# Performance work log

Measured on AMD Instinct MI355X. Metric: run time of the kernel, lower is better.

The kernel has to match this reference:

```python
import jax, jax.numpy as jnp
import numpy as np

VOCAB = 1024
D = 1024  # predictor_dim
B = 32
U = 512
NULL_INDEX = 0


def setup_inputs() -> dict:
    key = jax.random.key(0)
    ks = jax.random.split(key, 9)
    s = 1.0 / np.sqrt(D)
    return {
        "y": jax.random.randint(ks[0], (B, U), 0, VOCAB, dtype=jnp.int32),
        "embed_table": jax.random.normal(ks[1], (VOCAB, D), jnp.float32) * s,
        "Wx": jax.random.normal(ks[2], (D, 3 * D), jnp.float32) * s,  # input kernel [z|r|h]
        "Wh": jax.random.normal(ks[3], (D, 3 * D), jnp.float32) * s,  # recurrent kernel [z|r|h]
        "bx": jnp.zeros((3 * D,), jnp.float32),  # input bias (reset_after=True)
        "bh": jnp.zeros((3 * D,), jnp.float32),  # recurrent bias (reset_after=True)
        "Wd": jax.random.normal(ks[4], (D, D), jnp.float32) * s,
        "bd": jnp.zeros((D,), jnp.float32),
        "h0": jax.random.normal(ks[5], (D,), jnp.float32),  # self.initial_state
    }


def _gru_scan(tokens, embed_table, Wx, Wh, bx, bh, h0_b):
    # tokens: [B, T] int; returns hidden states [B, T, D]
    x = embed_table[tokens]                       # [B, T, D]
    # Precompute all input projections outside the recurrence (one big GEMM)
    xp = jnp.einsum("btd,de->bte", x, Wx) + bx    # [B, T, 3D]
    xp = jnp.moveaxis(xp, 1, 0)                   # [T, B, 3D]

    def step(h, xp_t):
        hp = h @ Wh + bh                          # [B, 3D], reset_after=True
        xz, xr, xh = jnp.split(xp_t, 3, axis=-1)
        hz, hr, hh = jnp.split(hp, 3, axis=-1)
        z = jax.nn.sigmoid(xz + hz)
        r = jax.nn.sigmoid(xr + hr)
        hcand = jnp.tanh(xh + r * hh)
        h_new = z * h + (1.0 - z) * hcand
        return h_new, h_new

    _, hs = jax.lax.scan(step, h0_b, xp)          # hs: [T, B, D]
    return jnp.moveaxis(hs, 0, 1)                 # [B, T, D]


def reference(y, embed_table, Wx, Wh, bx, bh, Wd, bd, h0):
    Bn = y.shape[0]
    start = jnp.full((Bn, 1), NULL_INDEX, dtype=y.dtype)
    tokens = jnp.concatenate([start, y], axis=1)  # [B, U+1]
    h0_b = jnp.broadcast_to(h0, (Bn, D))
    hs = _gru_scan(tokens, embed_table, Wx, Wh, bx, bh, h0_b)  # [B, U+1, D]
    outs = jnp.einsum("btd,de->bte", hs, Wd) + bd
    return outs
```

## Files before the change

### kernel.cpp

```cpp
#include <hip/hip_runtime.h>
#include <hip/hip_bf16.h>
#include <cstdint>

typedef __bf16 bf16;
typedef __bf16 bf16x8 __attribute__((ext_vector_type(8)));
typedef float  f32x4  __attribute__((ext_vector_type(4)));
typedef uint32_t u32x4 __attribute__((ext_vector_type(4)));

#define D_DIM   1024
#define ND      3072
#define B_SZ    32
#define U_SZ    512
#define T_SZ    513
#define M_REAL  (B_SZ * T_SZ)
#define WXS_LD  1032
#define A_LD    1032

#define AGENT __HIP_MEMORY_SCOPE_AGENT

__device__ __forceinline__ f32x4 mfma16(bf16x8 a, bf16x8 b, f32x4 c) {
    return __builtin_amdgcn_mfma_f32_16x16x32_bf16(a, b, c, 0, 0, 0);
}

struct bfpair { bf16x8 hi, lo; };

__device__ __forceinline__ bfpair split8(const float* p) {
    f32x4 a = *(const f32x4*)p;
    f32x4 b = *(const f32x4*)(p + 4);
    bfpair r;
#pragma unroll
    for (int j = 0; j < 4; ++j) {
        r.hi[j] = (bf16)a[j];
        r.lo[j] = (bf16)(a[j] - (float)r.hi[j]);
        r.hi[4 + j] = (bf16)b[j];
        r.lo[4 + j] = (bf16)(b[j] - (float)r.hi[4 + j]);
    }
    return r;
}

__device__ __forceinline__ bf16x8 cvt8(const float* p) {
    f32x4 a = *(const f32x4*)p;
    f32x4 b = *(const f32x4*)(p + 4);
    bf16x8 r;
#pragma unroll
    for (int j = 0; j < 4; ++j) { r[j] = (bf16)a[j]; r[4 + j] = (bf16)b[j]; }
    return r;
}

__device__ __forceinline__ bfpair unpack8(const uint32_t* p) {
    u32x4 a = *(const u32x4*)p;
    u32x4 b = *(const u32x4*)(p + 4);
    union { uint32_t u[4]; bf16x8 v; } H, L;
    H.u[0] = __builtin_amdgcn_perm(a.y, a.x, 0x05040100u);
    H.u[1] = __builtin_amdgcn_perm(a.w, a.z, 0x05040100u);
    H.u[2] = __builtin_amdgcn_perm(b.y, b.x, 0x05040100u);
    H.u[3] = __builtin_amdgcn_perm(b.w, b.z, 0x05040100u);
    L.u[0] = __builtin_amdgcn_perm(a.y, a.x, 0x07060302u);
    L.u[1] = __builtin_amdgcn_perm(a.w, a.z, 0x07060302u);
    L.u[2] = __builtin_amdgcn_perm(b.y, b.x, 0x07060302u);
    L.u[3] = __builtin_amdgcn_perm(b.w, b.z, 0x07060302u);
    bfpair r; r.hi = H.v; r.lo = L.v;
    return r;
}

__global__ void transpose_split(const float* __restrict__ in,
                                bf16* __restrict__ out_hi, bf16* __restrict__ out_lo,
                                int R, int C) {
    __shared__ float tile[32][33];
    const int c0 = blockIdx.x * 32, r0 = blockIdx.y * 32;
    const int tx = threadIdx.x, ty = threadIdx.y;
    for (int i = 0; i < 32; i += 8)
        tile[ty + i][tx] = in[(size_t)(r0 + ty + i) * C + c0 + tx];
    __syncthreads();
    for (int i = 0; i < 32; i += 8) {
        const float v  = tile[tx][ty + i];
        const bf16  hi = (bf16)v;
        const int col = c0 + ty + i;
        const int row = r0 + tx;
        const size_t idx = ((size_t)((col >> 4) * 32 + (row >> 5)) << 9)
                         + (((row >> 3) & 3) << 7) + ((col & 15) << 3) + (row & 7);
        out_hi[idx] = hi;
        out_lo[idx] = (bf16)(v - (float)hi);
    }
}

__global__ __launch_bounds__(256, 1)
void gru_scan(const float* __restrict__ Wx,    const float* __restrict__ Wh,
              const float* __restrict__ bx,    const float* __restrict__ bh,
              const float* __restrict__ h0,    const float* __restrict__ embed,
              const int* __restrict__ y,       uint32_t* __restrict__ ghs,
              int* __restrict__ flags)
{
    __shared__ __align__(16) bf16 WxS[48 * WXS_LD];
    __shared__ float hpx[48 * 17];
    __shared__ float xpx[2][48 * 17];
    __shared__ float bhs[48], bxs[48];

    const int tid  = threadIdx.x;
    const int wave = tid >> 6, lane = tid & 63;
    const int quad = lane >> 4, l15 = lane & 15;
    const int mhalf = blockIdx.x & 1;
    const int n0 = (blockIdx.x >> 1) * 16;
    int* slots = flags;
    int* go    = flags + 512;

    for (int idx = tid; idx < 3 * 1024 * 16; idx += 256) {
        const int cl = idx & 15;
        const int k  = (idx >> 4) & 1023;
        const int g  = idx >> 14;
        WxS[(g * 16 + cl) * WXS_LD + k] = (bf16)Wx[(size_t)k * ND + g * D_DIM + n0 + cl];
    }
    if (tid < 48) {
        bhs[tid] = bh[(tid >> 4) * D_DIM + n0 + (tid & 15)];
        bxs[tid] = bx[(tid >> 4) * D_DIM + n0 + (tid & 15)];
    }

    bf16x8 breg[32];
    if (wave < 3) {
#pragma unroll
        for (int ks = 0; ks < 32; ++ks) {
            bf16x8 v;
#pragma unroll
            for (int j = 0; j < 8; ++j)
                v[j] = (bf16)Wh[(size_t)(ks * 32 + quad * 8 + j) * ND
                                + wave * D_DIM + n0 + l15];
            breg[ks] = v;
        }
    }

    const int gml = tid >> 4, nl = tid & 15;
    const int gb  = mhalf * 16 + gml;
    const int gn  = n0 + nl;
    float hold = h0[gn];
    uint32_t pkjunk = 0;

    __syncthreads();

    if (wave == 3) {
        const float* xrow = embed + quad * 8;
        f32x4 ax0 = {}, ax1 = {}, ax2 = {};
#pragma unroll
        for (int ks = 0; ks < 32; ++ks) {
            bf16x8 xa = cvt8(xrow + ks * 32);
            bf16x8 w0 = *(const bf16x8*)(WxS + (l15)      * WXS_LD + ks * 32 + quad * 8);
            bf16x8 w1 = *(const bf16x8*)(WxS + (16 + l15) * WXS_LD + ks * 32 + quad * 8);
            bf16x8 w2 = *(const bf16x8*)(WxS + (32 + l15) * WXS_LD + ks * 32 + quad * 8);
            ax0 = mfma16(xa, w0, ax0);
            ax1 = mfma16(xa, w1, ax1);
            ax2 = mfma16(xa, w2, ax2);
        }
#pragma unroll
        for (int i = 0; i < 4; ++i) {
            xpx[0][(quad * 4 + i) * 17 + l15]      = ax0[i];
            xpx[0][(16 + quad * 4 + i) * 17 + l15] = ax1[i];
            xpx[0][(32 + quad * 4 + i) * 17 + l15] = ax2[i];
        }
    }

    for (int t = 0; t < T_SZ; ++t) {
        if (wave < 3) {
            f32x4 a0 = {}, a1 = {};
            if (t == 0) {
                const float* hrow = h0 + quad * 8;
#pragma unroll
                for (int ks = 0; ks < 32; ++ks) {
                    bfpair h8 = split8(hrow + ks * 32);
                    a0 = mfma16(h8.hi, breg[ks], a0);
                    a1 = mfma16(h8.lo, breg[ks], a1);
                }
            } else {
                const uint32_t* hrow = ghs
                    + ((size_t)(mhalf * 16 + l15) * T_SZ + (t - 1)) * D_DIM + quad * 8;
#pragma unroll
                for (int ks = 0; ks < 32; ++ks) {
                    bfpair h8 = unpack8(hrow + ks * 32);
                    a0 = mfma16(h8.hi, breg[ks], a0);
                    a1 = mfma16(h8.lo, breg[ks], a1);
                }
            }
            a0 = a0 + a1;
#pragma unroll
            for (int i = 0; i < 4; ++i)
                hpx[(wave * 16 + quad * 4 + i) * 17 + l15] = a0[i];
        }

        if (wave == 3 && t < U_SZ) {
            const int tok = y[(mhalf * 16 + l15) * U_SZ + t] & 1023;
            const float* xrow = embed + (size_t)tok * D_DIM + quad * 8;
            const int p = (t + 1) & 1;
            f32x4 ax0 = {}, ax1 = {}, ax2 = {};
#pragma unroll
            for (int ks = 0; ks < 32; ++ks) {
                bf16x8 xa = cvt8(xrow + ks * 32);
                bf16x8 w0 = *(const bf16x8*)(WxS + (l15)      * WXS_LD + ks * 32 + quad * 8);
                bf16x8 w1 = *(const bf16x8*)(WxS + (16 + l15) * WXS_LD + ks * 32 + quad * 8);
                bf16x8 w2 = *(const bf16x8*)(WxS + (32 + l15) * WXS_LD + ks * 32 + quad * 8);
                ax0 = mfma16(xa, w0, ax0);
                ax1 = mfma16(xa, w1, ax1);
                ax2 = mfma16(xa, w2, ax2);
            }
#pragma unroll
            for (int i = 0; i < 4; ++i) {
                xpx[p][(quad * 4 + i) * 17 + l15]      = ax0[i];
                xpx[p][(16 + quad * 4 + i) * 17 + l15] = ax1[i];
                xpx[p][(32 + quad * 4 + i) * 17 + l15] = ax2[i];
            }
        }
        __syncthreads();

        {
            const int p = t & 1;
            const float xz = xpx[p][(gml)      * 17 + nl] + bxs[nl];
            const float xr = xpx[p][(16 + gml) * 17 + nl] + bxs[16 + nl];
            const float xh = xpx[p][(32 + gml) * 17 + nl] + bxs[32 + nl];
            const float hz = hpx[(gml)      * 17 + nl] + bhs[nl];
            const float hr = hpx[(16 + gml) * 17 + nl] + bhs[16 + nl];
            const float hh = hpx[(32 + gml) * 17 + nl] + bhs[32 + nl];
            const float z  = 1.f / (1.f + __expf(-(xz + hz)));
            const float r  = 1.f / (1.f + __expf(-(xr + hr)));
            const float pa = xh + r * hh;
            const float hc = 1.f - 2.f / (__expf(2.f * pa) + 1.f);
            const float hn = z * hold + (1.f - z) * hc;
            hold = hn;
            union { uint16_t u[2]; uint32_t w; } pk;
            const bf16 hi = (bf16)hn;
            const bf16 lo = (bf16)(hn - (float)hi);
            pk.u[0] = __builtin_bit_cast(uint16_t, hi);
            pk.u[1] = __builtin_bit_cast(uint16_t, lo);
            uint32_t old = __hip_atomic_exchange(
                ghs + ((size_t)gb * T_SZ + t) * D_DIM + gn, pk.w,
                __ATOMIC_RELAXED, AGENT);
            pkjunk ^= old;
        }

        if (t + 1 < T_SZ) {
            __syncthreads();
            const int tv = t + 1;
            if (blockIdx.x == 0) {
                if (wave == 0) {
                    int ok;
                    do {
                        const int s1 = __hip_atomic_load(slots + lane * 4,
                                                         __ATOMIC_RELAXED, AGENT);
                        const int s2 = __hip_atomic_load(slots + (lane + 64) * 4,
                                                         __ATOMIC_RELAXED, AGENT);
                        ok = (lane == 0 || s1 >= tv) && (s2 >= tv);
                    } while (!__all(ok));
                    if (lane < 8)
                        __hip_atomic_store(go + lane * 16, tv,
                                           __ATOMIC_RELAXED, AGENT);
                }
            } else {
                if (tid == 0) {
                    __hip_atomic_store(slots + blockIdx.x * 4, tv,
                                       __ATOMIC_RELAXED, AGENT);
                    while (__hip_atomic_load(go + (blockIdx.x & 7) * 16,
                                             __ATOMIC_RELAXED, AGENT) < tv) {}
                }
            }
            __syncthreads();
        }
    }

    if (pkjunk == 0xDEADBEEFu) flags[1023] = 1;
}

__global__ __launch_bounds__(256, 1)
void gemm_rows_inplace(float* __restrict__ C,
                       const bf16* __restrict__ WdTh, const bf16* __restrict__ WdTl,
                       const float* __restrict__ bd)
{
    __shared__ __align__(16) bf16 Ah[32 * A_LD];
    __shared__ __align__(16) bf16 Al[32 * A_LD];
    const int tid  = threadIdx.x;
    const int wave = tid >> 6, lane = tid & 63;
    const int quad = lane >> 4, l15 = lane & 15;
    const size_t r0 = (size_t)blockIdx.x * 32;
    const uint32_t* Cw = (const uint32_t*)C;

    for (int idx = tid; idx < 32 * 128; idx += 256) {
        const int r = idx >> 7, ch = idx & 127;
        bfpair p = unpack8(Cw + (r0 + r) * D_DIM + ch * 8);
        *(bf16x8*)(Ah + r * A_LD + ch * 8) = p.hi;
        *(bf16x8*)(Al + r * A_LD + ch * 8) = p.lo;
    }
    __syncthreads();

    f32x4 acc[2][16] = {};
    for (int ks = 0; ks < 32; ++ks) {
        bf16x8 a0h = *(const bf16x8*)(Ah + (l15)      * A_LD + ks * 32 + quad * 8);
        bf16x8 a0l = *(const bf16x8*)(Al + (l15)      * A_LD + ks * 32 + quad * 8);
        bf16x8 a1h = *(const bf16x8*)(Ah + (16 + l15) * A_LD + ks * 32 + quad * 8);
        bf16x8 a1l = *(const bf16x8*)(Al + (16 + l15) * A_LD + ks * 32 + quad * 8);
#pragma unroll
        for (int nt = 0; nt < 16; ++nt) {
            const int cg = wave * 16 + nt;
            const size_t boff = (((size_t)cg * 32 + ks) << 9) + (size_t)lane * 8;
            bf16x8 bhv = *(const bf16x8*)(WdTh + boff);
            bf16x8 blv = *(const bf16x8*)(WdTl + boff);
            acc[0][nt] = mfma16(a0h, bhv, acc[0][nt]);
            acc[0][nt] = mfma16(a0l, bhv, acc[0][nt]);
            acc[0][nt] = mfma16(a0h, blv, acc[0][nt]);
            acc[1][nt] = mfma16(a1h, bhv, acc[1][nt]);
            acc[1][nt] = mfma16(a1l, bhv, acc[1][nt]);
            acc[1][nt] = mfma16(a1h, blv, acc[1][nt]);
        }
    }

    const int nbase = wave * 256;
#pragma unroll
    for (int nt = 0; nt < 16; ++nt) {
        const int col = nbase + nt * 16 + l15;
        const float bvl = bd[col];
#pragma unroll
        for (int mt = 0; mt < 2; ++mt)
#pragma unroll
            for (int i = 0; i < 4; ++i)
                C[(r0 + mt * 16 + quad * 4 + i) * D_DIM + col] =
                    acc[mt][nt][i] + bvl;
    }
}

extern "C" void kernel_launch(void* const* d_in, const int* in_sizes, int n_in,
                              void* d_out, int out_size, void* d_ws, size_t ws_size,
                              hipStream_t stream) {
    (void)in_sizes; (void)n_in; (void)out_size; (void)ws_size;
    const int*   y     = (const int*)  d_in[0];
    const float* embed = (const float*)d_in[1];
    const float* Wx    = (const float*)d_in[2];
    const float* Wh    = (const float*)d_in[3];
    const float* bx    = (const float*)d_in[4];
    const float* bh    = (const float*)d_in[5];
    const float* Wd    = (const float*)d_in[6];
    const float* bd    = (const float*)d_in[7];
    const float* h0    = (const float*)d_in[8];
    float* out = (float*)d_out;

    bf16* WdTh = (bf16*)d_ws;
    bf16* WdTl = WdTh + (size_t)D_DIM * D_DIM;
    int* flags = (int*)((char*)d_ws + (size_t)D_DIM * D_DIM * 4);

    hipMemsetAsync(flags, 0, 8192, stream);

    transpose_split<<<dim3(D_DIM / 32, D_DIM / 32), dim3(32, 8), 0, stream>>>(
        Wd, WdTh, WdTl, D_DIM, D_DIM);

    gru_scan<<<128, 256, 0, stream>>>(Wx, Wh, bx, bh, h0, embed, y,
                                      (uint32_t*)out, flags);

    gemm_rows_inplace<<<M_REAL / 32, 256, 0, stream>>>(out, WdTh, WdTl, bd);
}
```

Measured before the change: 7.317 ms.

## Retile output GEMM to 64-row blocks loading packed A directly from global

```diff
diff --git a/kernel.cpp b/kernel.cpp
--- a/kernel.cpp
+++ b/kernel.cpp
@@ -14,7 +14,6 @@
 #define T_SZ    513
 #define M_REAL  (B_SZ * T_SZ)
 #define WXS_LD  1032
-#define A_LD    1032
 
 #define AGENT __HIP_MEMORY_SCOPE_AGENT
 
@@ -265,59 +264,66 @@
     if (pkjunk == 0xDEADBEEFu) flags[1023] = 1;
 }
 
-__global__ __launch_bounds__(256, 1)
+__global__ __launch_bounds__(512, 1)
 void gemm_rows_inplace(float* __restrict__ C,
                        const bf16* __restrict__ WdTh, const bf16* __restrict__ WdTl,
                        const float* __restrict__ bd)
 {
-    __shared__ __align__(16) bf16 Ah[32 * A_LD];
-    __shared__ __align__(16) bf16 Al[32 * A_LD];
     const int tid  = threadIdx.x;
     const int wave = tid >> 6, lane = tid & 63;
     const int quad = lane >> 4, l15 = lane & 15;
-    const size_t r0 = (size_t)blockIdx.x * 32;
+    const size_t r0 = (size_t)blockIdx.x * 64;
     const uint32_t* Cw = (const uint32_t*)C;
 
-    for (int idx = tid; idx < 32 * 128; idx += 256) {
-        const int r = idx >> 7, ch = idx & 127;
-        bfpair p = unpack8(Cw + (r0 + r) * D_DIM + ch * 8);
-        *(bf16x8*)(Ah + r * A_LD + ch * 8) = p.hi;
-        *(bf16x8*)(Al + r * A_LD + ch * 8) = p.lo;
-    }
-    __syncthreads();
-
-    f32x4 acc[2][16] = {};
+    int rows[4];
+#pragma unroll
+    for (int mt = 0; mt < 4; ++mt) {
+        int r = (int)r0 + mt * 16 + l15;
+        rows[mt] = (r < M_REAL) ? r : (M_REAL - 1);
+    }
+
+    f32x4 acc[4][8] = {};
     for (int ks = 0; ks < 32; ++ks) {
-        bf16x8 a0h = *(const bf16x8*)(Ah + (l15)      * A_LD + ks * 32 + quad * 8);
-        bf16x8 a0l = *(const bf16x8*)(Al + (l15)      * A_LD + ks * 32 + quad * 8);
-        bf16x8 a1h = *(const bf16x8*)(Ah + (16 + l15) * A_LD + ks * 32 + quad * 8);
-        bf16x8 a1l = *(const bf16x8*)(Al + (16 + l15) * A_LD + ks * 32 + quad * 8);
-#pragma unroll
-        for (int nt = 0; nt < 16; ++nt) {
-            const int cg = wave * 16 + nt;
+        bfpair a0 = unpack8(Cw + (size_t)rows[0] * D_DIM + ks * 32 + quad * 8);
+        bfpair a1 = unpack8(Cw + (size_t)rows[1] * D_DIM + ks * 32 + quad * 8);
+        bfpair a2 = unpack8(Cw + (size_t)rows[2] * D_DIM + ks * 32 + quad * 8);
+        bfpair a3 = unpack8(Cw + (size_t)rows[3] * D_DIM + ks * 32 + quad * 8);
+#pragma unroll
+        for (int nt = 0; nt < 8; ++nt) {
+            const int cg = wave * 8 + nt;
             const size_t boff = (((size_t)cg * 32 + ks) << 9) + (size_t)lane * 8;
             bf16x8 bhv = *(const bf16x8*)(WdTh + boff);
             bf16x8 blv = *(const bf16x8*)(WdTl + boff);
-            acc[0][nt] = mfma16(a0h, bhv, acc[0][nt]);
-            acc[0][nt] = mfma16(a0l, bhv, acc[0][nt]);
-            acc[0][nt] = mfma16(a0h, blv, acc[0][nt]);
-            acc[1][nt] = mfma16(a1h, bhv, acc[1][nt]);
-            acc[1][nt] = mfma16(a1l, bhv, acc[1][nt]);
-            acc[1][nt] = mfma16(a1h, blv, acc[1][nt]);
-        }
-    }
-
-    const int nbase = wave * 256;
-#pragma unroll
-    for (int nt = 0; nt < 16; ++nt) {
-        const int col = nbase + nt * 16 + l15;
+            acc[0][nt] = mfma16(a0.hi, bhv, acc[0][nt]);
+            acc[0][nt] = mfma16(a0.lo, bhv, acc[0][nt]);
+            acc[0][nt] = mfma16(a0.hi, blv, acc[0][nt]);
+            acc[1][nt] = mfma16(a1.hi, bhv, acc[1][nt]);
+            acc[1][nt] = mfma16(a1.lo, bhv, acc[1][nt]);
+            acc[1][nt] = mfma16(a1.hi, blv, acc[1][nt]);
+            acc[2][nt] = mfma16(a2.hi, bhv, acc[2][nt]);
+            acc[2][nt] = mfma16(a2.lo, bhv, acc[2][nt]);
+            acc[2][nt] = mfma16(a2.hi, blv, acc[2][nt]);
+            acc[3][nt] = mfma16(a3.hi, bhv, acc[3][nt]);
+            acc[3][nt] = mfma16(a3.lo, bhv, acc[3][nt]);
+            acc[3][nt] = mfma16(a3.hi, blv, acc[3][nt]);
+        }
+    }
+
+    __syncthreads();
+
+#pragma unroll
+    for (int nt = 0; nt < 8; ++nt) {
+        const int col = wave * 128 + nt * 16 + l15;
         const float bvl = bd[col];
 #pragma unroll
-        for (int mt = 0; mt < 2; ++mt)
-#pragma unroll
-            for (int i = 0; i < 4; ++i)
-                C[(r0 + mt * 16 + quad * 4 + i) * D_DIM + col] =
-                    acc[mt][nt][i] + bvl;
+        for (int mt = 0; mt < 4; ++mt) {
+#pragma unroll
+            for (int i = 0; i < 4; ++i) {
+                const size_t row = r0 + mt * 16 + quad * 4 + i;
+                if (row < M_REAL)
+                    C[row * D_DIM + col] = acc[mt][nt][i] + bvl;
+            }
+        }
     }
 }
 
@@ -348,5 +354,5 @@
     gru_scan<<<128, 256, 0, stream>>>(Wx, Wh, bx, bh, h0, embed, y,
                                       (uint32_t*)out, flags);
 
-    gemm_rows_inplace<<<M_REAL / 32, 256, 0, stream>>>(out, WdTh, WdTl, bd);
-}
+    gemm_rows_inplace<<<(M_REAL + 63) / 64, 512, 0, stream>>>(out, WdTh, WdTl, bd);
+}
```

Result: no change. 7.205 ms, median of 3 (-1.5%).
